# Kernel optimization log

Hardware: AMD Instinct MI355X
Metric: run time of the kernel (lower is better)

Reference implementation:

```python
import jax, jax.numpy as jnp
import numpy as np

B, S, D, O, R, E = 4, 2048, 4096, 4096, 16, 8
SCALING = 32.0 / 16.0  # lora_alpha / lora_rank


def setup_inputs() -> dict:
    key = jax.random.key(0)
    ks = jax.random.split(key, 7)
    x = jax.random.normal(ks[0], (B, S, D), dtype=jnp.float32)
    W_base = jax.random.normal(ks[1], (O, D), dtype=jnp.float32) * 0.02
    b_base = jnp.zeros((O,), dtype=jnp.float32)
    A_w = jax.random.normal(ks[2], (R, D), dtype=jnp.float32) * 0.02     # lora_A weight
    B_w = jax.random.normal(ks[3], (O, R), dtype=jnp.float32) * 0.02     # lora_B weight
    router_w = jax.random.normal(ks[4], (E, D), dtype=jnp.float32) * 0.02  # router weight (core_router=False -> acts on x)
    cores = jax.random.normal(ks[5], (E, R, R), dtype=jnp.float32)       # expert rank x rank cores
    return {"x": x, "W_base": W_base, "b_base": b_base, "A_w": A_w,
            "B_w": B_w, "router_w": router_w, "cores": cores}


def reference(x, W_base, b_base, A_w, B_w, router_w, cores):
    # base linear: [B,S,O]
    result = jnp.einsum('bsd,od->bso', x, W_base) + b_base
    # lora down-projection (dropout=0 -> identity): [B,S,R]
    ax = jnp.einsum('bsd,rd->bsr', x, A_w)
    # router on x (core_router=False): softmax over experts -> [B,S,E]
    probs = jax.nn.softmax(jnp.einsum('bsd,ed->bse', x, router_w), axis=-1)
    # per-token weighted core applied to ax WITHOUT materializing [B,S,R,R]:
    # first ax through each expert core [B,S,E,R], then weight-reduce over experts.
    per_expert = jnp.einsum('bsr,erq->bseq', ax, cores)
    mixed = jnp.einsum('bseq,bse->bsq', per_expert, probs)  # [B,S,R]
    result = result + jnp.einsum('bsr,or->bso', mixed, B_w) * SCALING
    return result
```

## Files before the change

### kernel.cpp

```cpp
#include <hip/hip_runtime.h>
#include <stdint.h>

#define D_DIM 4096
#define O_DIM 4096
#define M_DIM 8192
#define BK 32
#define NKT 128

typedef __attribute__((ext_vector_type(4))) float f32x4;
typedef __attribute__((ext_vector_type(8))) __bf16 bf16x8;
typedef __attribute__((ext_vector_type(8))) unsigned short u16x8;

__device__ __forceinline__ unsigned short f32_to_bf16_bits(float f) {
    union { float f; uint32_t u; } v; v.f = f;
    return (unsigned short)((v.u + 0x7FFFu + ((v.u >> 16) & 1u)) >> 16);
}

__device__ __forceinline__ float dot4(f32x4 a, f32x4 b) {
    return fmaf(a.x, b.x, fmaf(a.y, b.y, fmaf(a.z, b.z, a.w * b.w)));
}

__device__ __forceinline__ int swz(int b) { return b ^ (((b >> 7) & 7) << 4); }

__global__ __launch_bounds__(256) void pre_kernel(const float* __restrict__ x,
                                                  const float* __restrict__ W_base,
                                                  const float* __restrict__ A_w,
                                                  const float* __restrict__ router_w,
                                                  unsigned short* __restrict__ xbf,
                                                  unsigned short* __restrict__ wbf,
                                                  float* __restrict__ ypart) {
    __shared__ __align__(16) float Xc[32][132];
    __shared__ __align__(16) float Wc[24][132];

    const int tid = threadIdx.x;

    {
        const int base = blockIdx.x * 2048;
        #pragma unroll
        for (int i = 0; i < 8; ++i) {
            const int idx = base + i * 256 + tid;
            f32x4 v = ((const f32x4*)W_base)[idx];
            ushort4 o;
            o.x = f32_to_bf16_bits(v.x);
            o.y = f32_to_bf16_bits(v.y);
            o.z = f32_to_bf16_bits(v.z);
            o.w = f32_to_bf16_bits(v.w);
            ((ushort4*)wbf)[idx] = o;
        }
    }

    const int tile = blockIdx.x & 255;
    const int ds = blockIdx.x >> 8;
    const int d0 = ds * 512;

    const int tok0 = tile * 32;
    const int tg = tid >> 3;
    const int og = tid & 7;
    float acc0 = 0.f, acc1 = 0.f, acc2 = 0.f;

    for (int sub = 0; sub < 4; ++sub) {
        const int dbase = d0 + sub * 128;
        __syncthreads();
        #pragma unroll
        for (int i = 0; i < 4; ++i) {
            int idx = i * 256 + tid;
            int t = idx >> 5, dq = idx & 31;
            f32x4 v = *(const f32x4*)&x[(size_t)(tok0 + t) * D_DIM + dbase + dq * 4];
            *(f32x4*)&Xc[t][dq * 4] = v;
            ushort4 o;
            o.x = f32_to_bf16_bits(v.x);
            o.y = f32_to_bf16_bits(v.y);
            o.z = f32_to_bf16_bits(v.z);
            o.w = f32_to_bf16_bits(v.w);
            *(ushort4*)&xbf[(size_t)(tok0 + t) * D_DIM + dbase + dq * 4] = o;
        }
        #pragma unroll
        for (int i = 0; i < 3; ++i) {
            int idx = i * 256 + tid;
            int r = idx >> 5, dq = idx & 31;
            const float* src = (r < 16) ? (A_w + (size_t)r * D_DIM)
                                        : (router_w + (size_t)(r - 16) * D_DIM);
            *(f32x4*)&Wc[r][dq * 4] = *(const f32x4*)&src[dbase + dq * 4];
        }
        __syncthreads();
        #pragma unroll
        for (int dq = 0; dq < 32; ++dq) {
            f32x4 xv = *(const f32x4*)&Xc[tg][dq * 4];
            acc0 += dot4(xv, *(const f32x4*)&Wc[og * 3 + 0][dq * 4]);
            acc1 += dot4(xv, *(const f32x4*)&Wc[og * 3 + 1][dq * 4]);
            acc2 += dot4(xv, *(const f32x4*)&Wc[og * 3 + 2][dq * 4]);
        }
    }
    float* dst = ypart + (((size_t)ds * 256 + tile) * 32 + tg) * 24 + og * 3;
    dst[0] = acc0; dst[1] = acc1; dst[2] = acc2;
}

__global__ __launch_bounds__(128) void fin_kernel(const float* __restrict__ ypart,
                                                  const float* __restrict__ cores,
                                                  const float* __restrict__ Bw,
                                                  unsigned short* __restrict__ mixbf,
                                                  unsigned short* __restrict__ bwbf) {
    const int tid = threadIdx.x;

    if (blockIdx.x >= 64) {
        const int o = (blockIdx.x - 64) * 128 + tid;
        ushort4* dst = (ushort4*)&bwbf[(size_t)o * 32];
        #pragma unroll
        for (int g = 0; g < 4; ++g) {
            f32x4 v = *(const f32x4*)&Bw[(size_t)o * 16 + g * 4];
            ushort4 u;
            u.x = f32_to_bf16_bits(v.x);
            u.y = f32_to_bf16_bits(v.y);
            u.z = f32_to_bf16_bits(v.z);
            u.w = f32_to_bf16_bits(v.w);
            dst[g] = u;
        }
        const ushort4 z = {0, 0, 0, 0};
        #pragma unroll
        for (int g = 4; g < 8; ++g) dst[g] = z;
        return;
    }

    __shared__ __align__(16) float Cs[2048];
    #pragma unroll
    for (int i = 0; i < 4; ++i) {
        int idx = i * 128 + tid;
        ((f32x4*)Cs)[idx] = ((const f32x4*)cores)[idx];
    }
    __syncthreads();

    const int tok = blockIdx.x * 128 + tid;
    const int tile = tok >> 5, t = tok & 31;

    float y[24];
    #pragma unroll
    for (int j = 0; j < 24; ++j) y[j] = 0.f;
    for (int ds = 0; ds < 8; ++ds) {
        const float* src = ypart + (((size_t)ds * 256 + tile) * 32 + t) * 24;
        #pragma unroll
        for (int j = 0; j < 24; ++j) y[j] += src[j];
    }

    float mx = y[16];
    #pragma unroll
    for (int e = 1; e < 8; ++e) mx = fmaxf(mx, y[16 + e]);
    float p[8], psum = 0.f;
    #pragma unroll
    for (int e = 0; e < 8; ++e) { p[e] = __expf(y[16 + e] - mx); psum += p[e]; }
    const float inv = 1.0f / psum;

    float outq[16];
    #pragma unroll
    for (int q = 0; q < 16; ++q) outq[q] = 0.f;
    for (int e = 0; e < 8; ++e) {
        const float pe = p[e] * inv;
        #pragma unroll
        for (int r = 0; r < 16; ++r) {
            const float ar = y[r] * pe;
            #pragma unroll
            for (int q = 0; q < 16; ++q)
                outq[q] = fmaf(ar, Cs[(e * 16 + r) * 16 + q], outq[q]);
        }
    }
    ushort4* dst = (ushort4*)&mixbf[(size_t)tok * 32];
    #pragma unroll
    for (int g = 0; g < 4; ++g) {
        ushort4 u;
        u.x = f32_to_bf16_bits(2.0f * outq[g * 4 + 0]);
        u.y = f32_to_bf16_bits(2.0f * outq[g * 4 + 1]);
        u.z = f32_to_bf16_bits(2.0f * outq[g * 4 + 2]);
        u.w = f32_to_bf16_bits(2.0f * outq[g * 4 + 3]);
        dst[g] = u;
    }
    const ushort4 z = {0, 0, 0, 0};
    #pragma unroll
    for (int g = 4; g < 8; ++g) dst[g] = z;
}

__global__ __launch_bounds__(512, 2) void gemm_kernel(const unsigned short* __restrict__ xbf,
                                                      const unsigned short* __restrict__ wbf,
                                                      const float* __restrict__ bias,
                                                      const unsigned short* __restrict__ mixbf,
                                                      const unsigned short* __restrict__ bwbf,
                                                      float* __restrict__ out) {
    __shared__ __align__(16) unsigned short lds[4][2][256 * 32];

    const int bid = blockIdx.x;
    const int xcd = bid & 7;
    const int lid = bid >> 3;
    const int tm = (lid >> 4) * 8 + xcd;
    const int tn = lid & 15;
    const int m0 = tm * 256, n0 = tn * 256;

    const int tid = threadIdx.x;
    const int wave = tid >> 6, lane = tid & 63;
    const int wr = wave >> 2, wcn = wave & 3;

    int aoff[2], boff[2], mmoff[2], mboff[2];
    #pragma unroll
    for (int u = 0; u < 2; ++u) {
        int c = u * 512 + tid;
        int g = swz(c * 16);
        int grow = g >> 6, gc8 = (g >> 4) & 3;
        aoff[u] = (m0 + grow) * D_DIM + gc8 * 8;
        boff[u] = (n0 + grow) * D_DIM + gc8 * 8;
        mmoff[u] = (m0 + grow) * 32 + gc8 * 8;
        mboff[u] = (n0 + grow) * 32 + gc8 * 8;
    }

    const int tA = lane & 15, kq = lane >> 4;
    int aRd[8], bRd[4];
    #pragma unroll
    for (int mi = 0; mi < 8; ++mi)
        aRd[mi] = swz((wr * 128 + mi * 16 + tA) * 64 + kq * 16);
    #pragma unroll
    for (int ni = 0; ni < 4; ++ni)
        bRd[ni] = swz((wcn * 64 + ni * 16 + tA) * 64 + kq * 16);

    f32x4 acc[8][4];
    const f32x4 fz = {0.f, 0.f, 0.f, 0.f};
    #pragma unroll
    for (int mi = 0; mi < 8; ++mi)
        #pragma unroll
        for (int ni = 0; ni < 4; ++ni) acc[mi][ni] = fz;

#define STAGE_UNIT(sb, kt, u, isA)                                                        \
    do {                                                                                  \
        const unsigned short* gsrc =                                                      \
            (isA) ? (xbf + aoff[u] + (kt)*BK) : (wbf + boff[u] + (kt)*BK);                \
        __builtin_amdgcn_global_load_lds(                                                 \
            (const __attribute__((address_space(1))) void*)gsrc,                          \
            (__attribute__((address_space(3))) void*)(&lds[sb][(isA) ? 0 : 1]             \
                                                         [((u)*512 + wave * 64) * 8]),    \
            16, 0, 0);                                                                    \
    } while (0)

#define STAGE_MIX(u, isA)                                                                 \
    do {                                                                                  \
        const unsigned short* gsrc = (isA) ? (mixbf + mmoff[u]) : (bwbf + mboff[u]);      \
        __builtin_amdgcn_global_load_lds(                                                 \
            (const __attribute__((address_space(1))) void*)gsrc,                          \
            (__attribute__((address_space(3))) void*)(&lds[0][(isA) ? 0 : 1]              \
                                                         [((u)*512 + wave * 64) * 8]),    \
            16, 0, 0);                                                                    \
    } while (0)

#define K_ITER(BUF, SBUF, KT, STG, VMC)                                                   \
    {                                                                                     \
        const char* Ab = (const char*)&lds[BUF][0][0];                                    \
        const char* Bb = (const char*)&lds[BUF][1][0];                                    \
        bf16x8 b0 = __builtin_bit_cast(bf16x8, *(const u16x8*)(Bb + bRd[0]));             \
        bf16x8 b1 = __builtin_bit_cast(bf16x8, *(const u16x8*)(Bb + bRd[1]));             \
        bf16x8 b2 = __builtin_bit_cast(bf16x8, *(const u16x8*)(Bb + bRd[2]));             \
        bf16x8 b3 = __builtin_bit_cast(bf16x8, *(const u16x8*)(Bb + bRd[3]));             \
        bf16x8 a0 = __builtin_bit_cast(bf16x8, *(const u16x8*)(Ab + aRd[0]));             \
        bf16x8 a1 = __builtin_bit_cast(bf16x8, *(const u16x8*)(Ab + aRd[1]));             \
        bf16x8 a2 = __builtin_bit_cast(bf16x8, *(const u16x8*)(Ab + aRd[2]));             \
        bf16x8 a3 = __builtin_bit_cast(bf16x8, *(const u16x8*)(Ab + aRd[3]));             \
        if (STG) {                                                                        \
            STAGE_UNIT(SBUF, KT, 0, 1);                                                   \
            STAGE_UNIT(SBUF, KT, 1, 1);                                                   \
        }                                                                                 \
        asm volatile("" ::: "memory");                                                    \
        __builtin_amdgcn_s_barrier();                                                     \
        asm volatile("" ::: "memory");                                                    \
        __builtin_amdgcn_s_setprio(1);                                                    \
        acc[0][0] = __builtin_amdgcn_mfma_f32_16x16x32_bf16(a0, b0, acc[0][0], 0, 0, 0);  \
        acc[0][1] = __builtin_amdgcn_mfma_f32_16x16x32_bf16(a0, b1, acc[0][1], 0, 0, 0);  \
        acc[0][2] = __builtin_amdgcn_mfma_f32_16x16x32_bf16(a0, b2, acc[0][2], 0, 0, 0);  \
        acc[0][3] = __builtin_amdgcn_mfma_f32_16x16x32_bf16(a0, b3, acc[0][3], 0, 0, 0);  \
        acc[1][0] = __builtin_amdgcn_mfma_f32_16x16x32_bf16(a1, b0, acc[1][0], 0, 0, 0);  \
        acc[1][1] = __builtin_amdgcn_mfma_f32_16x16x32_bf16(a1, b1, acc[1][1], 0, 0, 0);  \
        acc[1][2] = __builtin_amdgcn_mfma_f32_16x16x32_bf16(a1, b2, acc[1][2], 0, 0, 0);  \
        acc[1][3] = __builtin_amdgcn_mfma_f32_16x16x32_bf16(a1, b3, acc[1][3], 0, 0, 0);  \
        acc[2][0] = __builtin_amdgcn_mfma_f32_16x16x32_bf16(a2, b0, acc[2][0], 0, 0, 0);  \
        acc[2][1] = __builtin_amdgcn_mfma_f32_16x16x32_bf16(a2, b1, acc[2][1], 0, 0, 0);  \
        acc[2][2] = __builtin_amdgcn_mfma_f32_16x16x32_bf16(a2, b2, acc[2][2], 0, 0, 0);  \
        acc[2][3] = __builtin_amdgcn_mfma_f32_16x16x32_bf16(a2, b3, acc[2][3], 0, 0, 0);  \
        acc[3][0] = __builtin_amdgcn_mfma_f32_16x16x32_bf16(a3, b0, acc[3][0], 0, 0, 0);  \
        acc[3][1] = __builtin_amdgcn_mfma_f32_16x16x32_bf16(a3, b1, acc[3][1], 0, 0, 0);  \
        acc[3][2] = __builtin_amdgcn_mfma_f32_16x16x32_bf16(a3, b2, acc[3][2], 0, 0, 0);  \
        acc[3][3] = __builtin_amdgcn_mfma_f32_16x16x32_bf16(a3, b3, acc[3][3], 0, 0, 0);  \
        __builtin_amdgcn_s_setprio(0);                                                    \
        asm volatile("" ::: "memory");                                                    \
        __builtin_amdgcn_s_barrier();                                                     \
        asm volatile("" ::: "memory");                                                    \
        bf16x8 a4 = __builtin_bit_cast(bf16x8, *(const u16x8*)(Ab + aRd[4]));             \
        bf16x8 a5 = __builtin_bit_cast(bf16x8, *(const u16x8*)(Ab + aRd[5]));             \
        bf16x8 a6 = __builtin_bit_cast(bf16x8, *(const u16x8*)(Ab + aRd[6]));             \
        bf16x8 a7 = __builtin_bit_cast(bf16x8, *(const u16x8*)(Ab + aRd[7]));             \
        if (STG) {                                                                        \
            STAGE_UNIT(SBUF, KT, 0, 0);                                                   \
            STAGE_UNIT(SBUF, KT, 1, 0);                                                   \
        }                                                                                 \
        asm volatile("s_waitcnt vmcnt(" #VMC ")" ::: "memory");                           \
        __builtin_amdgcn_s_barrier();                                                     \
        asm volatile("" ::: "memory");                                                    \
        __builtin_amdgcn_s_setprio(1);                                                    \
        acc[4][0] = __builtin_amdgcn_mfma_f32_16x16x32_bf16(a4, b0, acc[4][0], 0, 0, 0);  \
        acc[4][1] = __builtin_amdgcn_mfma_f32_16x16x32_bf16(a4, b1, acc[4][1], 0, 0, 0);  \
        acc[4][2] = __builtin_amdgcn_mfma_f32_16x16x32_bf16(a4, b2, acc[4][2], 0, 0, 0);  \
        acc[4][3] = __builtin_amdgcn_mfma_f32_16x16x32_bf16(a4, b3, acc[4][3], 0, 0, 0);  \
        acc[5][0] = __builtin_amdgcn_mfma_f32_16x16x32_bf16(a5, b0, acc[5][0], 0, 0, 0);  \
        acc[5][1] = __builtin_amdgcn_mfma_f32_16x16x32_bf16(a5, b1, acc[5][1], 0, 0, 0);  \
        acc[5][2] = __builtin_amdgcn_mfma_f32_16x16x32_bf16(a5, b2, acc[5][2], 0, 0, 0);  \
        acc[5][3] = __builtin_amdgcn_mfma_f32_16x16x32_bf16(a5, b3, acc[5][3], 0, 0, 0);  \
        acc[6][0] = __builtin_amdgcn_mfma_f32_16x16x32_bf16(a6, b0, acc[6][0], 0, 0, 0);  \
        acc[6][1] = __builtin_amdgcn_mfma_f32_16x16x32_bf16(a6, b1, acc[6][1], 0, 0, 0);  \
        acc[6][2] = __builtin_amdgcn_mfma_f32_16x16x32_bf16(a6, b2, acc[6][2], 0, 0, 0);  \
        acc[6][3] = __builtin_amdgcn_mfma_f32_16x16x32_bf16(a6, b3, acc[6][3], 0, 0, 0);  \
        acc[7][0] = __builtin_amdgcn_mfma_f32_16x16x32_bf16(a7, b0, acc[7][0], 0, 0, 0);  \
        acc[7][1] = __builtin_amdgcn_mfma_f32_16x16x32_bf16(a7, b1, acc[7][1], 0, 0, 0);  \
        acc[7][2] = __builtin_amdgcn_mfma_f32_16x16x32_bf16(a7, b2, acc[7][2], 0, 0, 0);  \
        acc[7][3] = __builtin_amdgcn_mfma_f32_16x16x32_bf16(a7, b3, acc[7][3], 0, 0, 0);  \
        __builtin_amdgcn_s_setprio(0);                                                    \
        asm volatile("s_waitcnt lgkmcnt(0)" ::: "memory");                                \
        __builtin_amdgcn_s_barrier();                                                     \
        asm volatile("" ::: "memory");                                                    \
    }

    #pragma unroll
    for (int kt = 0; kt < 3; ++kt) {
        STAGE_UNIT(kt, kt, 0, 1);
        STAGE_UNIT(kt, kt, 1, 1);
        STAGE_UNIT(kt, kt, 0, 0);
        STAGE_UNIT(kt, kt, 1, 0);
    }
    asm volatile("s_waitcnt vmcnt(8)" ::: "memory");
    __builtin_amdgcn_s_barrier();
    asm volatile("" ::: "memory");

    for (int jj = 0; jj < 31; ++jj) {
        #pragma unroll
        for (int i = 0; i < 4; ++i) {
            const int j = jj * 4 + i;
            const int kt = j + 3;
            K_ITER(i, (i + 3) & 3, kt, 1, 8);
        }
    }
    K_ITER(0, 3, 127, 1, 8);
    K_ITER(1, 0, 0, 0, 4);
    K_ITER(2, 0, 0, 0, 0);
    K_ITER(3, 0, 0, 0, 0);

    STAGE_MIX(0, 1);
    STAGE_MIX(1, 1);
    STAGE_MIX(0, 0);
    STAGE_MIX(1, 0);
    asm volatile("s_waitcnt vmcnt(0)" ::: "memory");
    __builtin_amdgcn_s_barrier();
    asm volatile("" ::: "memory");
    K_ITER(0, 0, 0, 0, 0);
#undef K_ITER
#undef STAGE_MIX
#undef STAGE_UNIT

    const int colq = lane & 15, rq = lane >> 4;
    float bcol[4];
    #pragma unroll
    for (int ni = 0; ni < 4; ++ni) bcol[ni] = bias[n0 + wcn * 64 + ni * 16 + colq];
    #pragma unroll
    for (int mi = 0; mi < 8; ++mi) {
        #pragma unroll
        for (int j = 0; j < 4; ++j) {
            const int row = m0 + wr * 128 + mi * 16 + rq * 4 + j;
            #pragma unroll
            for (int ni = 0; ni < 4; ++ni) {
                const int col = n0 + wcn * 64 + ni * 16 + colq;
                out[(size_t)row * O_DIM + col] = acc[mi][ni][j] + bcol[ni];
            }
        }
    }
}

extern "C" void kernel_launch(void* const* d_in, const int* in_sizes, int n_in,
                              void* d_out, int out_size, void* d_ws, size_t ws_size,
                              hipStream_t stream) {
    const float* x        = (const float*)d_in[0];
    const float* W_base   = (const float*)d_in[1];
    const float* b_base   = (const float*)d_in[2];
    const float* A_w      = (const float*)d_in[3];
    const float* B_w      = (const float*)d_in[4];
    const float* router_w = (const float*)d_in[5];
    const float* cores    = (const float*)d_in[6];
    float* out = (float*)d_out;

    char* ws = (char*)d_ws;
    unsigned short* xbf = (unsigned short*)ws;
    unsigned short* wbf = (unsigned short*)(ws + (size_t)M_DIM * D_DIM * 2);
    char* p = ws + (size_t)M_DIM * D_DIM * 2 + (size_t)O_DIM * D_DIM * 2;
    unsigned short* mixbf = (unsigned short*)p;
    unsigned short* bwbf  = (unsigned short*)(p + (size_t)M_DIM * 32 * 2);
    float* ypart = (float*)(p + (size_t)M_DIM * 32 * 2 + (size_t)O_DIM * 32 * 2);

    pre_kernel<<<2048, 256, 0, stream>>>(x, W_base, A_w, router_w, xbf, wbf, ypart);
    fin_kernel<<<96, 128, 0, stream>>>(ypart, cores, B_w, mixbf, bwbf);
    gemm_kernel<<<512, 512, 0, stream>>>(xbf, wbf, b_base, mixbf, bwbf, out);
}
```

Baseline: 340.1 us.

## Split weight conversion into its own kernel and register-tile the LoRA/router projection

Moves the W_base fp32-to-bf16 conversion out of the fused pre-kernel into a separate grid-stride kernel. The x·[A;router] projection now gives each thread 4 tokens by 3 weight rows over a quarter of the D chunk, so each shared-memory weight load is reused across several tokens. The four partial sums per output are then combined through shared memory. This is meant to cut LDS traffic per FMA in the small projection, at the cost of an extra kernel launch and an extra reduction phase with added barriers.

```diff
diff --git a/kernel.cpp b/kernel.cpp
--- a/kernel.cpp
+++ b/kernel.cpp
@@ -22,41 +22,43 @@
 
 __device__ __forceinline__ int swz(int b) { return b ^ (((b >> 7) & 7) << 4); }
 
-__global__ __launch_bounds__(256) void pre_kernel(const float* __restrict__ x,
-                                                  const float* __restrict__ W_base,
-                                                  const float* __restrict__ A_w,
-                                                  const float* __restrict__ router_w,
-                                                  unsigned short* __restrict__ xbf,
-                                                  unsigned short* __restrict__ wbf,
-                                                  float* __restrict__ ypart) {
+__global__ __launch_bounds__(256) void convert_bf16_kernel(const float* __restrict__ src,
+                                                           unsigned short* __restrict__ dst,
+                                                           int n4) {
+    int stride = gridDim.x * blockDim.x;
+    for (int i = blockIdx.x * blockDim.x + threadIdx.x; i < n4; i += stride) {
+        f32x4 v = ((const f32x4*)src)[i];
+        ushort4 o;
+        o.x = f32_to_bf16_bits(v.x);
+        o.y = f32_to_bf16_bits(v.y);
+        o.z = f32_to_bf16_bits(v.z);
+        o.w = f32_to_bf16_bits(v.w);
+        ((ushort4*)dst)[i] = o;
+    }
+}
+
+__global__ __launch_bounds__(256) void partial_mixed_kernel(const float* __restrict__ x,
+                                                            const float* __restrict__ A_w,
+                                                            const float* __restrict__ router_w,
+                                                            unsigned short* __restrict__ xbf,
+                                                            float* __restrict__ ypart) {
     __shared__ __align__(16) float Xc[32][132];
     __shared__ __align__(16) float Wc[24][132];
 
     const int tid = threadIdx.x;
-
-    {
-        const int base = blockIdx.x * 2048;
-        #pragma unroll
-        for (int i = 0; i < 8; ++i) {
-            const int idx = base + i * 256 + tid;
-            f32x4 v = ((const f32x4*)W_base)[idx];
-            ushort4 o;
-            o.x = f32_to_bf16_bits(v.x);
-            o.y = f32_to_bf16_bits(v.y);
-            o.z = f32_to_bf16_bits(v.z);
-            o.w = f32_to_bf16_bits(v.w);
-            ((ushort4*)wbf)[idx] = o;
-        }
-    }
-
-    const int tile = blockIdx.x & 255;
-    const int ds = blockIdx.x >> 8;
-    const int d0 = ds * 512;
-
-    const int tok0 = tile * 32;
-    const int tg = tid >> 3;
-    const int og = tid & 7;
-    float acc0 = 0.f, acc1 = 0.f, acc2 = 0.f;
+    const int t0 = blockIdx.x * 32;
+    const int d0 = blockIdx.y * 512;
+
+    const int slot = tid & 63;
+    const int q = tid >> 6;
+    const int tg4 = slot >> 3;
+    const int og = slot & 7;
+
+    float acc[4][3];
+    #pragma unroll
+    for (int ti = 0; ti < 4; ++ti)
+        #pragma unroll
+        for (int wi = 0; wi < 3; ++wi) acc[ti][wi] = 0.f;
 
     for (int sub = 0; sub < 4; ++sub) {
         const int dbase = d0 + sub * 128;
@@ -65,14 +67,14 @@
         for (int i = 0; i < 4; ++i) {
             int idx = i * 256 + tid;
             int t = idx >> 5, dq = idx & 31;
-            f32x4 v = *(const f32x4*)&x[(size_t)(tok0 + t) * D_DIM + dbase + dq * 4];
+            f32x4 v = *(const f32x4*)&x[(size_t)(t0 + t) * D_DIM + dbase + dq * 4];
             *(f32x4*)&Xc[t][dq * 4] = v;
             ushort4 o;
             o.x = f32_to_bf16_bits(v.x);
             o.y = f32_to_bf16_bits(v.y);
             o.z = f32_to_bf16_bits(v.z);
             o.w = f32_to_bf16_bits(v.w);
-            *(ushort4*)&xbf[(size_t)(tok0 + t) * D_DIM + dbase + dq * 4] = o;
+            *(ushort4*)&xbf[(size_t)(t0 + t) * D_DIM + dbase + dq * 4] = o;
         }
         #pragma unroll
         for (int i = 0; i < 3; ++i) {
@@ -84,15 +86,40 @@
         }
         __syncthreads();
         #pragma unroll
-        for (int dq = 0; dq < 32; ++dq) {
-            f32x4 xv = *(const f32x4*)&Xc[tg][dq * 4];
-            acc0 += dot4(xv, *(const f32x4*)&Wc[og * 3 + 0][dq * 4]);
-            acc1 += dot4(xv, *(const f32x4*)&Wc[og * 3 + 1][dq * 4]);
-            acc2 += dot4(xv, *(const f32x4*)&Wc[og * 3 + 2][dq * 4]);
-        }
-    }
-    float* dst = ypart + (((size_t)ds * 256 + tile) * 32 + tg) * 24 + og * 3;
-    dst[0] = acc0; dst[1] = acc1; dst[2] = acc2;
+        for (int dqi = 0; dqi < 8; ++dqi) {
+            const int dq = q * 8 + dqi;
+            f32x4 w0 = *(const f32x4*)&Wc[og * 3 + 0][dq * 4];
+            f32x4 w1 = *(const f32x4*)&Wc[og * 3 + 1][dq * 4];
+            f32x4 w2 = *(const f32x4*)&Wc[og * 3 + 2][dq * 4];
+            #pragma unroll
+            for (int ti = 0; ti < 4; ++ti) {
+                f32x4 xv = *(const f32x4*)&Xc[tg4 * 4 + ti][dq * 4];
+                acc[ti][0] += dot4(xv, w0);
+                acc[ti][1] += dot4(xv, w1);
+                acc[ti][2] += dot4(xv, w2);
+            }
+        }
+    }
+
+    __syncthreads();
+    float* red = &Xc[0][0];
+    #pragma unroll
+    for (int ti = 0; ti < 4; ++ti)
+        #pragma unroll
+        for (int wi = 0; wi < 3; ++wi)
+            red[(slot * 4 + q) * 12 + ti * 3 + wi] = acc[ti][wi];
+    __syncthreads();
+    #pragma unroll
+    for (int k = 0; k < 3; ++k) {
+        const int flat = tid * 3 + k;
+        const int t = flat / 24, j = flat % 24;
+        const int s = ((t >> 2) << 3) | (j / 3);
+        const int ti = t & 3, wi = j % 3;
+        float v = 0.f;
+        #pragma unroll
+        for (int qq = 0; qq < 4; ++qq) v += red[(s * 4 + qq) * 12 + ti * 3 + wi];
+        ypart[(((size_t)blockIdx.y * 256 + blockIdx.x) * 32 + t) * 24 + j] = v;
+    }
 }
 
 __global__ __launch_bounds__(128) void fin_kernel(const float* __restrict__ ypart,
@@ -393,7 +420,8 @@
     unsigned short* bwbf  = (unsigned short*)(p + (size_t)M_DIM * 32 * 2);
     float* ypart = (float*)(p + (size_t)M_DIM * 32 * 2 + (size_t)O_DIM * 32 * 2);
 
-    pre_kernel<<<2048, 256, 0, stream>>>(x, W_base, A_w, router_w, xbf, wbf, ypart);
+    convert_bf16_kernel<<<2048, 256, 0, stream>>>(W_base, wbf, (O_DIM * D_DIM) / 4);
+    partial_mixed_kernel<<<dim3(256, 8), 256, 0, stream>>>(x, A_w, router_w, xbf, ypart);
     fin_kernel<<<96, 128, 0, stream>>>(ypart, cores, B_w, mixbf, bwbf);
     gemm_kernel<<<512, 512, 0, stream>>>(xbf, wbf, b_base, mixbf, bwbf, out);
 }
```

After: 325.8 us (median of 3 runs). 1.04x faster.
